# Kernel optimization log

Measured on AMD Instinct MI355X. Metric: run time of the kernel, lower is better.

## Reference

```python
import jax, jax.numpy as jnp
import numpy as np
from jax import lax

HEADS = 4
DIM = 64
GATE_HID = 16


def setup_inputs() -> dict:
    key = jax.random.key(0)
    ks = jax.random.split(key, 12)
    b, c, h, w = 2, DIM, 48, 48
    s = 0.05
    x = jax.random.normal(ks[0], (b, c, h, w), jnp.float32)
    Wqkv = jax.random.normal(ks[1], (3 * c, c), jnp.float32) * s
    bqkv = jax.random.normal(ks[2], (3 * c,), jnp.float32) * s
    Wpos = jax.random.normal(ks[3], (3 * c, 1, 3, 3), jnp.float32) * s
    bpos = jax.random.normal(ks[4], (3 * c,), jnp.float32) * s
    Wg1 = jax.random.normal(ks[5], (GATE_HID, 1), jnp.float32) * 0.5
    bg1 = jax.random.normal(ks[6], (GATE_HID,), jnp.float32) * 0.1
    Wg2 = jax.random.normal(ks[7], (1, GATE_HID), jnp.float32) * 0.5
    bg2 = jax.random.normal(ks[8], (1,), jnp.float32) * 0.1
    Wproj = jax.random.normal(ks[9], (c, c), jnp.float32) * s
    bproj = jax.random.normal(ks[10], (c,), jnp.float32) * s
    return {"x": x, "Wqkv": Wqkv, "bqkv": bqkv, "Wpos": Wpos, "bpos": bpos,
            "Wg1": Wg1, "bg1": bg1, "Wg2": Wg2, "bg2": bg2,
            "Wproj": Wproj, "bproj": bproj}


def _forward(x, Wqkv, bqkv, Wpos, bpos, Wg1, bg1, Wg2, bg2, Wproj, bproj):
    b, c, h, w = x.shape
    n = h * w
    heads = HEADS
    hd = c // heads
    scale = hd ** -0.5
    # qkv 1x1 conv then 3x3 depthwise positional conv
    qkv = jnp.einsum('bchw,oc->bohw', x, Wqkv) + bqkv[None, :, None, None]
    qkv = lax.conv_general_dilated(
        qkv, Wpos, window_strides=(1, 1), padding='SAME',
        feature_group_count=3 * c,
        dimension_numbers=('NCHW', 'OIHW', 'NCHW')) + bpos[None, :, None, None]
    q, k, v = jnp.split(qkv, 3, axis=1)

    def to_heads(t):
        # [b,c,h,w] -> [b,heads,n,hd]
        return t.reshape(b, c, n).transpose(0, 2, 1).reshape(b, n, heads, hd).transpose(0, 2, 1, 3)

    q, k, v = to_heads(q), to_heads(k), to_heads(v)
    attn = jnp.einsum('bhid,bhjd->bhij', q, k) * scale  # [b,heads,n,n]
    prob = jax.nn.softmax(attn, axis=-1)
    entropy = -(prob * jnp.log(jnp.clip(prob, 1e-12))).sum(-1).mean(-1)  # [b,heads]
    # entropy gate: sigmoid(fc2(relu(fc1(e)))) * 0.9 + 0.1
    hgate = jax.nn.relu(entropy[..., None] @ Wg1.T + bg1)  # [b,heads,16]
    ratio = jax.nn.sigmoid(hgate @ Wg2.T + bg2)[..., 0] * 0.9 + 0.1  # [b,heads]
    # dynamic per-(batch,head) top-k along rows via rank threshold
    keep = jnp.clip(jnp.ceil(ratio * n).astype(jnp.int32), 1, n)  # [b,heads]
    sorted_desc = -jnp.sort(-attn, axis=-1)  # [b,heads,n,n]
    idx = jnp.broadcast_to((keep - 1)[:, :, None, None], (b, heads, n, 1))
    thresh = jnp.take_along_axis(sorted_desc, idx, axis=-1)  # [b,heads,n,1]
    sparse = jnp.where(attn >= thresh, attn, -jnp.inf)
    p = jax.nn.softmax(sparse, axis=-1)
    out = jnp.einsum('bhij,bhjd->bhid', p, v)  # [b,heads,n,hd]
    out = out.transpose(0, 2, 1, 3).reshape(b, n, c)
    out = out @ Wproj.T + bproj
    return out.transpose(0, 2, 1).reshape(b, c, h, w)


def reference(x, Wqkv, bqkv, Wpos, bpos, Wg1, bg1, Wg2, bg2, Wproj, bproj):
    return _forward(x, Wqkv, bqkv, Wpos, bpos, Wg1, bg1, Wg2, bg2, Wproj, bproj)
```

## Files before the change

kernel.cpp:

```cpp
#include <hip/hip_runtime.h>
#include <hip/hip_fp16.h>


typedef _Float16 half8_t __attribute__((ext_vector_type(8)));
typedef float floatx4 __attribute__((ext_vector_type(4)));

union HU { unsigned short s; _Float16 h; };
__device__ __forceinline__ _Float16 ubits_h(unsigned short u) {
  HU c; c.s = u; return c.h;
}
__device__ __forceinline__ _Float16 key_h(unsigned k) {
  unsigned short u = (k & 0x8000u) ? (unsigned short)(k & 0x7FFFu)
                                   : (unsigned short)((~k) & 0xFFFFu);
  return ubits_h(u);
}

__device__ __forceinline__ uint2 hist_select_p(const unsigned* h, int lane,
                                               unsigned keepN) {
  uint2 w = ((const uint2*)h)[lane];
  unsigned c0 = w.x & 0xFFFFu, c1 = w.x >> 16;
  unsigned c2 = w.y & 0xFFFFu, c3 = w.y >> 16;
  unsigned inc = c0 + c1 + c2 + c3;
#pragma unroll
  for (int off = 1; off < 64; off <<= 1) {
    unsigned t = __shfl_up(inc, off);
    if (lane >= off) inc += t;
  }
  unsigned total = __shfl(inc, 63);
  unsigned above = total - inc;
  unsigned a3 = above;
  unsigned a2 = a3 + c3;
  unsigned a1 = a2 + c2;
  unsigned a0 = a1 + c1;
  bool has = false;
  unsigned B_l = 0, A_l = 0;
  if (a3 < keepN && a3 + c3 >= keepN) { has = true; B_l = lane * 4 + 3; A_l = a3; }
  else if (a2 < keepN && a2 + c2 >= keepN) { has = true; B_l = lane * 4 + 2; A_l = a2; }
  else if (a1 < keepN && a1 + c1 >= keepN) { has = true; B_l = lane * 4 + 1; A_l = a1; }
  else if (a0 < keepN && a0 + c0 >= keepN) { has = true; B_l = lane * 4 + 0; A_l = a0; }
  unsigned long long m = __ballot(has);
  int src = __ffsll(m) - 1;
  return make_uint2(__shfl(B_l, src), __shfl(A_l, src));
}

__global__ __launch_bounds__(256) void k_qkv(const float* __restrict__ x,
                                             const float* __restrict__ W,
                                             const float* __restrict__ bias,
                                             float* __restrict__ out,
                                             float* __restrict__ ent) {
  if (blockIdx.x == 0 && threadIdx.x < 8) ent[threadIdx.x] = 0.f;
  int blk = blockIdx.x;
  int chunk = blk % 9;
  int og = (blk / 9) % 48;
  int b = blk / (9 * 48);
  int o0 = og * 4;
  int pos = chunk * 256 + threadIdx.x;
  const float* xb = x + b * 64 * 2304 + pos;
  const float* w0 = W + (o0 + 0) * 64;
  const float* w1 = W + (o0 + 1) * 64;
  const float* w2 = W + (o0 + 2) * 64;
  const float* w3 = W + (o0 + 3) * 64;
  float a0 = bias[o0 + 0], a1 = bias[o0 + 1];
  float a2 = bias[o0 + 2], a3 = bias[o0 + 3];
#pragma unroll
  for (int c = 0; c < 64; c++) {
    float xv = xb[c * 2304];
    a0 = fmaf(w0[c], xv, a0);
    a1 = fmaf(w1[c], xv, a1);
    a2 = fmaf(w2[c], xv, a2);
    a3 = fmaf(w3[c], xv, a3);
  }
  out[(b * 192 + o0 + 0) * 2304 + pos] = a0;
  out[(b * 192 + o0 + 1) * 2304 + pos] = a1;
  out[(b * 192 + o0 + 2) * 2304 + pos] = a2;
  out[(b * 192 + o0 + 3) * 2304 + pos] = a3;
}

__global__ __launch_bounds__(256) void k_dw(const float* __restrict__ qkv,
                                            const float* __restrict__ Wpos,
                                            const float* __restrict__ bpos,
                                            _Float16* __restrict__ q2,
                                            _Float16* __restrict__ k2,
                                            _Float16* __restrict__ vt) {
  __shared__ float smem[8][384];
  int blk = blockIdx.x;
  int chunk = blk % 9;
  int half = (blk / 9) % 2;
  int sel = (blk / 18) % 3;
  int head = (blk / 54) % 4;
  int b = blk / 216;
  int chbase = sel * 64 + head * 16 + half * 8;
  int bh = b * 4 + head;
  int tid = threadIdx.x;
  int p0 = chunk * 256;
  int baserow = p0 / 48;
  int rA = min(max(baserow - 1, 0), 40);

  const float* src = qkv + (size_t)(b * 192 + chbase) * 2304;
#pragma unroll
  for (int l = 0; l < 12; l++) {
    int idx = tid + l * 256;
    int ch = idx / 384;
    int off = idx - ch * 384;
    int rr = off / 48;
    int cc = off - rr * 48;
    smem[ch][off] = src[(size_t)ch * 2304 + (rA + rr) * 48 + cc];
  }
  __syncthreads();

  int pos = p0 + tid;
  int yy = pos / 48, xx = pos - yy * 48;
  int ry = yy - rA;
  float accv[8];
#pragma unroll
  for (int d = 0; d < 8; d++) {
    const float* w = Wpos + (chbase + d) * 9;
    float a = bpos[chbase + d];
#pragma unroll
    for (int dy = -1; dy <= 1; dy++) {
      int y2 = yy + dy;
      if ((unsigned)y2 < 48u) {
#pragma unroll
        for (int dx = -1; dx <= 1; dx++) {
          int x2 = xx + dx;
          if ((unsigned)x2 < 48u)
            a = fmaf(w[(dy + 1) * 3 + (dx + 1)], smem[d][(ry + dy) * 48 + x2],
                     a);
        }
      }
    }
    accv[d] = a;
  }

  if (sel == 2) {
#pragma unroll
    for (int d = 0; d < 8; d++)
      vt[((size_t)bh * 16 + half * 8 + d) * 2304 + pos] = (_Float16)accv[d];
  } else {
    _Float16 h1[8], h2[8];
#pragma unroll
    for (int d = 0; d < 8; d++) {
      float a = (sel == 0) ? accv[d] * 0.25f : accv[d];
      h1[d] = (_Float16)a;
      h2[d] = (_Float16)(a - (float)h1[d]);
    }
    _Float16* dst = ((sel == 0) ? q2 : k2) + ((size_t)bh * 2304 + pos) * 32;
    *(uint4*)(dst + half * 8) = *(uint4*)&h1[0];
    *(uint4*)(dst + 16 + half * 8) = *(uint4*)&h2[0];
  }
}

template <bool STORE>
__global__ __launch_bounds__(256) void k_ent_t(const _Float16* __restrict__ q2,
                                               const _Float16* __restrict__ k2,
                                               float* __restrict__ ent,
                                               _Float16* __restrict__ lgH) {
  __shared__ __align__(16) _Float16 tBuf[4][16][72];
  __shared__ float sWv[4][16], uWv[4][16];

  int blk = blockIdx.x;
  int rowtile = blk % 144;
  int bh = blk / 144;
  int row0 = rowtile * 16;
  int tid = threadIdx.x, lane = tid & 63, wave = tid >> 6;
  int m16 = lane & 15, quad = lane >> 4;

  const half8_t* q2v =
      (const half8_t*)(q2 + ((size_t)bh * 2304 + row0 + m16) * 32);
  half8_t A1 = q2v[quad];
  half8_t zh = {};
  half8_t A2 = (lane < 32) ? A1 : zh;
  const half8_t* kbase = (const half8_t*)(k2 + (size_t)bh * 2304 * 32);

  float s[4] = {0.f, 0.f, 0.f, 0.f}, u[4] = {0.f, 0.f, 0.f, 0.f};
  for (int g = 0; g < 9; g++) {
#pragma unroll
    for (int tt = 0; tt < 4; tt++) {
      int t = g * 4 + tt;
      int col = wave * 576 + t * 16 + m16;
      const half8_t* kk = kbase + (size_t)col * 4;
      half8_t b1 = kk[quad & 1];
      half8_t b2 = kk[2 + (quad & 1)];
      floatx4 acc = {};
      acc = __builtin_amdgcn_mfma_f32_16x16x32_f16(A2, b2, acc, 0, 0, 0);
      acc = __builtin_amdgcn_mfma_f32_16x16x32_f16(A1, b1, acc, 0, 0, 0);
#pragma unroll
      for (int i = 0; i < 4; i++) {
        if (STORE) tBuf[wave][quad * 4 + i][tt * 16 + m16] = (_Float16)acc[i];
        float e = __expf(acc[i]);
        s[i] += e;
        u[i] = fmaf(acc[i], e, u[i]);
      }
    }
    if (STORE) {
      __syncthreads();
      int rb = lane >> 3, seg = lane & 7;
#pragma unroll
      for (int it = 0; it < 2; it++) {
        int rr = it * 8 + rb;
        uint4 vv = *(const uint4*)&tBuf[wave][rr][seg * 8];
        *(uint4*)(lgH + ((size_t)bh * 2304 + row0 + rr) * 2304 + wave * 576 +
                  g * 64 + seg * 8) = vv;
      }
      __syncthreads();
    }
  }
#pragma unroll
  for (int off = 1; off < 16; off <<= 1) {
#pragma unroll
    for (int i = 0; i < 4; i++) {
      s[i] += __shfl_xor(s[i], off);
      u[i] += __shfl_xor(u[i], off);
    }
  }
  if (m16 == 0) {
#pragma unroll
    for (int i = 0; i < 4; i++) {
      sWv[wave][quad * 4 + i] = s[i];
      uWv[wave][quad * 4 + i] = u[i];
    }
  }
  __syncthreads();
  if (tid < 16) {
    float S = sWv[0][tid] + sWv[1][tid] + sWv[2][tid] + sWv[3][tid];
    float U = uWv[0][tid] + uWv[1][tid] + uWv[2][tid] + uWv[3][tid];
    float er = __logf(S) - U / S;
    er += __shfl_xor(er, 1);
    er += __shfl_xor(er, 2);
    er += __shfl_xor(er, 4);
    er += __shfl_xor(er, 8);
    if (tid == 0) atomicAdd(&ent[bh], er);
  }
}

__global__ __launch_bounds__(512, 2) void k_attn_f(
    const _Float16* __restrict__ q2, const _Float16* __restrict__ k2,
    const _Float16* __restrict__ vt, const float* __restrict__ ent,
    const float* __restrict__ Wg1, const float* __restrict__ bg1,
    const float* __restrict__ Wg2, const float* __restrict__ bg2,
    float* __restrict__ oh) {
  __shared__ __align__(16) _Float16 lg[16 * 2304];
  __shared__ unsigned hist[8][128];
  __shared__ float sS[16];

  int blk = blockIdx.x;
  int bh = blk & 7;
  int tile = blk >> 3;
  int row0 = tile * 16;
  int tid = threadIdx.x, lane = tid & 63, wave = tid >> 6;
  int m16 = lane & 15, quad = lane >> 4;
  char* lgc = (char*)lg;

  float eAvg = ent[bh] * (1.f / 2304.f);
  float gacc = bg2[0];
#pragma unroll
  for (int i = 0; i < 16; i++) {
    float h = fmaxf(fmaf(eAvg, Wg1[i], bg1[i]), 0.f);
    gacc = fmaf(h, Wg2[i], gacc);
  }
  float ratio = 0.9f / (1.f + __expf(-gacc)) + 0.1f;
  int kp = (int)ceilf(ratio * 2304.f);
  unsigned keep = (unsigned)min(max(kp, 1), 2304);

  {
    const half8_t* q2v =
        (const half8_t*)(q2 + ((size_t)bh * 2304 + row0 + m16) * 32);
    half8_t A1 = q2v[quad];
    half8_t zh = {};
    half8_t A2 = (lane < 32) ? A1 : zh;
    const half8_t* kbase = (const half8_t*)(k2 + (size_t)bh * 2304 * 32);
#pragma unroll 2
    for (int t = 0; t < 18; t++) {
      int col = wave * 288 + t * 16 + m16;
      const half8_t* kk = kbase + (size_t)col * 4;
      half8_t b1 = kk[quad & 1];
      half8_t b2 = kk[2 + (quad & 1)];
      floatx4 acc = {};
      acc = __builtin_amdgcn_mfma_f32_16x16x32_f16(A2, b2, acc, 0, 0, 0);
      acc = __builtin_amdgcn_mfma_f32_16x16x32_f16(A1, b1, acc, 0, 0, 0);
#pragma unroll
      for (int i = 0; i < 4; i++) {
        int row = quad * 4 + i;
        *(_Float16*)(lgc + row * 4608 +
                     ((col * 2) ^ (((row >> 2) & 3) << 5))) =
            (_Float16)acc[i];
      }
    }
  }
  __syncthreads();

#pragma unroll 1
  for (int rr = 0; rr < 2; rr++) {
    int r = wave * 2 + rr;
    char* rb = lgc + r * 4608;
    int sw = ((r >> 2) & 3) << 5;
    uint4 q0 = *(const uint4*)(rb + ((lane * 16) ^ sw));
    uint4 q1 = *(const uint4*)(rb + ((1024 + lane * 16) ^ sw));
    uint4 q2r = *(const uint4*)(rb + ((2048 + lane * 16) ^ sw));
    uint4 q3 = *(const uint4*)(rb + ((3072 + lane * 16) ^ sw));
    uint2 q4 = *(const uint2*)(rb + ((4096 + lane * 8) ^ sw));
    unsigned wb[18] = {q0.x, q0.y, q0.z, q0.w, q1.x, q1.y, q1.z, q1.w,
                       q2r.x, q2r.y, q2r.z, q2r.w, q3.x, q3.y, q3.z, q3.w,
                       q4.x, q4.y};
    unsigned kb[18];
#pragma unroll
    for (int i = 0; i < 18; i++)
      kb[i] = wb[i] ^ (((wb[i] >> 15) & 0x00010001u) * 0x7FFFu + 0x80008000u);

    unsigned* h = hist[wave];
    h[lane] = 0u;
    h[lane + 64] = 0u;
#pragma unroll
    for (int i = 0; i < 18; i++) {
      unsigned b1 = (kb[i] >> 8) & 0xFFu;
      unsigned b2 = kb[i] >> 24;
      atomicAdd(&h[b1 >> 1], 1u << ((b1 & 1) << 4));
      atomicAdd(&h[b2 >> 1], 1u << ((b2 & 1) << 4));
    }
    uint2 s1 = hist_select_p(h, lane, keep);
    unsigned B = s1.x;
    unsigned keep2 = keep - s1.y;

    h[lane] = 0u;
    h[lane + 64] = 0u;
#pragma unroll
    for (int i = 0; i < 18; i++) {
      unsigned klo = kb[i] & 0xFFFFu;
      unsigned khi = kb[i] >> 16;
      if ((klo >> 8) == B) {
        unsigned lb = klo & 0xFFu;
        atomicAdd(&h[lb >> 1], 1u << ((lb & 1) << 4));
      }
      if ((khi >> 8) == B) {
        unsigned lb = khi & 0xFFu;
        atomicAdd(&h[lb >> 1], 1u << ((lb & 1) << 4));
      }
    }
    uint2 s2 = hist_select_p(h, lane, keep2);
    _Float16 th_h = key_h((B << 8) | s2.x);

    float sp = 0.f;
#pragma unroll
    for (int g = 0; g < 4; g++) {
      uint4 o;
      unsigned ow[4];
#pragma unroll
      for (int wj = 0; wj < 4; wj++) {
        unsigned w = wb[g * 4 + wj];
        _Float16 hlo = ubits_h((unsigned short)(w & 0xFFFFu));
        _Float16 hhi = ubits_h((unsigned short)(w >> 16));
        float plo = (hlo >= th_h) ? __expf((float)hlo) : 0.f;
        float phi = (hhi >= th_h) ? __expf((float)hhi) : 0.f;
        __half2 hp = __floats2half2_rn(plo, phi);
        ow[wj] = *(unsigned*)&hp;
        if (wj == 0) sp += ((plo + phi));
      }
      o.x = ow[0]; o.y = ow[1]; o.z = ow[2]; o.w = ow[3];
      *(uint4*)(rb + (((g * 1024) + lane * 16) ^ sw)) = o;
      {
        _Float16 h2a = ubits_h((unsigned short)(wb[g * 4 + 1] & 0xFFFFu));
        _Float16 h2b = ubits_h((unsigned short)(wb[g * 4 + 1] >> 16));
        _Float16 h3a = ubits_h((unsigned short)(wb[g * 4 + 2] & 0xFFFFu));
        _Float16 h3b = ubits_h((unsigned short)(wb[g * 4 + 2] >> 16));
        _Float16 h4a = ubits_h((unsigned short)(wb[g * 4 + 3] & 0xFFFFu));
        _Float16 h4b = ubits_h((unsigned short)(wb[g * 4 + 3] >> 16));
        float p2 = (h2a >= th_h) ? __expf((float)h2a) : 0.f;
        float p3 = (h2b >= th_h) ? __expf((float)h2b) : 0.f;
        float p4 = (h3a >= th_h) ? __expf((float)h3a) : 0.f;
        float p5 = (h3b >= th_h) ? __expf((float)h3b) : 0.f;
        float p6 = (h4a >= th_h) ? __expf((float)h4a) : 0.f;
        float p7 = (h4b >= th_h) ? __expf((float)h4b) : 0.f;
        sp += (p2 + p3);
        sp += (p4 + p5) + (p6 + p7);
      }
    }
    {
      _Float16 h0 = ubits_h((unsigned short)(wb[16] & 0xFFFFu));
      _Float16 h1 = ubits_h((unsigned short)(wb[16] >> 16));
      _Float16 h2 = ubits_h((unsigned short)(wb[17] & 0xFFFFu));
      _Float16 h3 = ubits_h((unsigned short)(wb[17] >> 16));
      float p0 = (h0 >= th_h) ? __expf((float)h0) : 0.f;
      float p1 = (h1 >= th_h) ? __expf((float)h1) : 0.f;
      float p2 = (h2 >= th_h) ? __expf((float)h2) : 0.f;
      float p3 = (h3 >= th_h) ? __expf((float)h3) : 0.f;
      sp += (p0 + p1) + (p2 + p3);
      uint2 o;
      __half2 hp0 = __floats2half2_rn(p0, p1); o.x = *(unsigned*)&hp0;
      __half2 hp1 = __floats2half2_rn(p2, p3); o.y = *(unsigned*)&hp1;
      *(uint2*)(rb + ((4096 + lane * 8) ^ sw)) = o;
    }
#pragma unroll
    for (int off = 1; off < 64; off <<= 1) sp += __shfl_xor(sp, off);
    if (lane == 0) sS[r] = sp;
  }
  __syncthreads();

  floatx4 acc = {};
  if (wave < 4) {
    const _Float16* vrow = vt + ((size_t)bh * 16 + m16) * 2304;
    const char* pr = lgc + m16 * 4608;
    int sw2 = ((m16 >> 2) & 3) << 5;
    int jb0 = wave * 576 + quad * 8;
#pragma unroll 6
    for (int t = 0; t < 18; t++) {
      int jb = jb0 + t * 32;
      half8_t a2 = *(const half8_t*)(pr + ((jb * 2) ^ sw2));
      half8_t b2 = *(const half8_t*)&vrow[jb];
      acc = __builtin_amdgcn_mfma_f32_16x16x32_f16(a2, b2, acc, 0, 0, 0);
    }
  }
  __syncthreads();
  float* red = (float*)lg;
  if (wave < 4) {
#pragma unroll
    for (int i = 0; i < 4; i++)
      red[wave * 256 + (quad * 4 + i) * 16 + m16] = acc[i];
  }
  __syncthreads();
  if (tid < 256) {
    int r = tid >> 4;
    float s2 = red[0 * 256 + tid] + red[1 * 256 + tid] +
               red[2 * 256 + tid] + red[3 * 256 + tid];
    int d = tid & 15;
    oh[((size_t)(bh * 2304 + row0 + r)) * 16 + d] = s2 / sS[r];
  }
}

__global__ __launch_bounds__(256) void k_proj(const float* __restrict__ oh,
                                              const float* __restrict__ Wp,
                                              const float* __restrict__ bp,
                                              float* __restrict__ out) {
  int blk = blockIdx.x;
  int chunk = blk % 9;
  int cog = (blk / 9) % 16;
  int b = blk / (9 * 16);
  int co0 = cog * 4;
  int pos = chunk * 256 + threadIdx.x;
  float a0 = bp[co0 + 0], a1 = bp[co0 + 1], a2 = bp[co0 + 2], a3 = bp[co0 + 3];
#pragma unroll
  for (int head = 0; head < 4; head++) {
    const float4* op =
        (const float4*)(oh + ((size_t)((b * 4 + head) * 2304 + pos)) * 16);
#pragma unroll
    for (int p = 0; p < 4; p++) {
      float4 o4 = op[p];
#pragma unroll
      for (int i = 0; i < 4; i++) {
        const float* wr = Wp + (co0 + i) * 64 + head * 16 + p * 4;
        float* ai = (i == 0) ? &a0 : ((i == 1) ? &a1 : ((i == 2) ? &a2 : &a3));
        *ai = fmaf(wr[0], o4.x, *ai);
        *ai = fmaf(wr[1], o4.y, *ai);
        *ai = fmaf(wr[2], o4.z, *ai);
        *ai = fmaf(wr[3], o4.w, *ai);
      }
    }
  }
  out[(b * 64 + co0 + 0) * 2304 + pos] = a0;
  out[(b * 64 + co0 + 1) * 2304 + pos] = a1;
  out[(b * 64 + co0 + 2) * 2304 + pos] = a2;
  out[(b * 64 + co0 + 3) * 2304 + pos] = a3;
}

extern "C" void kernel_launch(void* const* d_in, const int* in_sizes, int n_in,
                              void* d_out, int out_size, void* d_ws,
                              size_t ws_size, hipStream_t stream) {
  const float* x    = (const float*)d_in[0];
  const float* Wqkv = (const float*)d_in[1];
  const float* bqkv = (const float*)d_in[2];
  const float* Wpos = (const float*)d_in[3];
  const float* bpos = (const float*)d_in[4];
  const float* Wg1  = (const float*)d_in[5];
  const float* bg1  = (const float*)d_in[6];
  const float* Wg2  = (const float*)d_in[7];
  const float* bg2  = (const float*)d_in[8];
  const float* Wpr  = (const float*)d_in[9];
  const float* bpr  = (const float*)d_in[10];
  float* out = (float*)d_out;

  char* base = (char*)d_ws;
  float* qkv_raw = (float*)base;
  float* oh = qkv_raw + 884736;
  float* ent = oh + 294912;
  _Float16* q2 = (_Float16*)(ent + 8);
  _Float16* k2 = q2 + 589824;
  _Float16* vt = k2 + 589824;

  hipLaunchKernelGGL(k_qkv, dim3(2 * 48 * 9), dim3(256), 0, stream,
                     x, Wqkv, bqkv, qkv_raw, ent);
  hipLaunchKernelGGL(k_dw, dim3(432), dim3(256), 0, stream,
                     qkv_raw, Wpos, bpos, q2, k2, vt);
  hipLaunchKernelGGL((k_ent_t<false>), dim3(8 * 144), dim3(256), 0, stream,
                     q2, k2, ent, (_Float16*)nullptr);
  hipLaunchKernelGGL(k_attn_f, dim3(1152), dim3(512), 0, stream,
                     q2, k2, vt, ent, Wg1, bg1, Wg2, bg2, oh);
  hipLaunchKernelGGL(k_proj, dim3(2 * 16 * 9), dim3(256), 0, stream,
                     oh, Wpr, bpr, out);
}
```

Measured before the change: 200.9 us.

## Shrink attention tile to 8 rows per block to raise occupancy

```diff
diff --git a/kernel.cpp b/kernel.cpp
--- a/kernel.cpp
+++ b/kernel.cpp
@@ -233,23 +233,23 @@
   }
 }
 
-__global__ __launch_bounds__(512, 2) void k_attn_f(
+__global__ __launch_bounds__(512, 6) void k_attn_f(
     const _Float16* __restrict__ q2, const _Float16* __restrict__ k2,
     const _Float16* __restrict__ vt, const float* __restrict__ ent,
     const float* __restrict__ Wg1, const float* __restrict__ bg1,
     const float* __restrict__ Wg2, const float* __restrict__ bg2,
     float* __restrict__ oh) {
-  __shared__ __align__(16) _Float16 lg[16 * 2304];
+  __shared__ __align__(16) _Float16 lg[8 * 2320];
   __shared__ unsigned hist[8][128];
-  __shared__ float sS[16];
+  __shared__ float sS[8];
+  __shared__ __align__(16) float redSh[8][64];
 
   int blk = blockIdx.x;
   int bh = blk & 7;
   int tile = blk >> 3;
-  int row0 = tile * 16;
+  int row0 = tile * 8;
   int tid = threadIdx.x, lane = tid & 63, wave = tid >> 6;
   int m16 = lane & 15, quad = lane >> 4;
-  char* lgc = (char*)lg;
 
   float eAvg = ent[bh] * (1.f / 2304.f);
   float gacc = bg2[0];
@@ -264,7 +264,7 @@
 
   {
     const half8_t* q2v =
-        (const half8_t*)(q2 + ((size_t)bh * 2304 + row0 + m16) * 32);
+        (const half8_t*)(q2 + ((size_t)bh * 2304 + row0 + (m16 & 7)) * 32);
     half8_t A1 = q2v[quad];
     half8_t zh = {};
     half8_t A2 = (lane < 32) ? A1 : zh;
@@ -278,27 +278,23 @@
       floatx4 acc = {};
       acc = __builtin_amdgcn_mfma_f32_16x16x32_f16(A2, b2, acc, 0, 0, 0);
       acc = __builtin_amdgcn_mfma_f32_16x16x32_f16(A1, b1, acc, 0, 0, 0);
-#pragma unroll
-      for (int i = 0; i < 4; i++) {
-        int row = quad * 4 + i;
-        *(_Float16*)(lgc + row * 4608 +
-                     ((col * 2) ^ (((row >> 2) & 3) << 5))) =
-            (_Float16)acc[i];
+      if (quad < 2) {
+#pragma unroll
+        for (int i = 0; i < 4; i++)
+          lg[(quad * 4 + i) * 2320 + col] = (_Float16)acc[i];
       }
     }
   }
   __syncthreads();
 
-#pragma unroll 1
-  for (int rr = 0; rr < 2; rr++) {
-    int r = wave * 2 + rr;
-    char* rb = lgc + r * 4608;
-    int sw = ((r >> 2) & 3) << 5;
-    uint4 q0 = *(const uint4*)(rb + ((lane * 16) ^ sw));
-    uint4 q1 = *(const uint4*)(rb + ((1024 + lane * 16) ^ sw));
-    uint4 q2r = *(const uint4*)(rb + ((2048 + lane * 16) ^ sw));
-    uint4 q3 = *(const uint4*)(rb + ((3072 + lane * 16) ^ sw));
-    uint2 q4 = *(const uint2*)(rb + ((4096 + lane * 8) ^ sw));
+  {
+    char* rb = (char*)lg + wave * 4640;
+    const uint4* s4 = (const uint4*)rb;
+    uint4 q0 = s4[lane];
+    uint4 q1 = s4[lane + 64];
+    uint4 q2r = s4[lane + 128];
+    uint4 q3 = s4[lane + 192];
+    uint2 q4 = *(const uint2*)(rb + 4096 + lane * 8);
     unsigned wb[18] = {q0.x, q0.y, q0.z, q0.w, q1.x, q1.y, q1.z, q1.w,
                        q2r.x, q2r.y, q2r.z, q2r.w, q3.x, q3.y, q3.z, q3.w,
                        q4.x, q4.y};
@@ -340,6 +336,7 @@
     _Float16 th_h = key_h((B << 8) | s2.x);
 
     float sp = 0.f;
+    uint4* prow4 = (uint4*)rb;
 #pragma unroll
     for (int g = 0; g < 4; g++) {
       uint4 o;
@@ -356,7 +353,7 @@
         if (wj == 0) sp += ((plo + phi));
       }
       o.x = ow[0]; o.y = ow[1]; o.z = ow[2]; o.w = ow[3];
-      *(uint4*)(rb + (((g * 1024) + lane * 16) ^ sw)) = o;
+      prow4[lane + g * 64] = o;
       {
         _Float16 h2a = ubits_h((unsigned short)(wb[g * 4 + 1] & 0xFFFFu));
         _Float16 h2b = ubits_h((unsigned short)(wb[g * 4 + 1] >> 16));
@@ -387,42 +384,40 @@
       uint2 o;
       __half2 hp0 = __floats2half2_rn(p0, p1); o.x = *(unsigned*)&hp0;
       __half2 hp1 = __floats2half2_rn(p2, p3); o.y = *(unsigned*)&hp1;
-      *(uint2*)(rb + ((4096 + lane * 8) ^ sw)) = o;
+      *(uint2*)(rb + 4096 + lane * 8) = o;
     }
 #pragma unroll
     for (int off = 1; off < 64; off <<= 1) sp += __shfl_xor(sp, off);
-    if (lane == 0) sS[r] = sp;
+    if (lane == 0) sS[wave] = sp;
   }
   __syncthreads();
 
-  floatx4 acc = {};
-  if (wave < 4) {
+  {
+    int g = wave >> 2;
+    int jq = wave & 3;
     const _Float16* vrow = vt + ((size_t)bh * 16 + m16) * 2304;
-    const char* pr = lgc + m16 * 4608;
-    int sw2 = ((m16 >> 2) & 3) << 5;
-    int jb0 = wave * 576 + quad * 8;
+    const _Float16* prow = lg + (size_t)(g * 4 + (m16 & 3)) * 2320;
+    int jb0 = jq * 576 + quad * 8;
+    floatx4 acc = {};
 #pragma unroll 6
     for (int t = 0; t < 18; t++) {
       int jb = jb0 + t * 32;
-      half8_t a2 = *(const half8_t*)(pr + ((jb * 2) ^ sw2));
+      half8_t a2 = *(const half8_t*)&prow[jb];
       half8_t b2 = *(const half8_t*)&vrow[jb];
       acc = __builtin_amdgcn_mfma_f32_16x16x32_f16(a2, b2, acc, 0, 0, 0);
     }
+    if (lane < 16) {
+      *(floatx4*)&redSh[wave][m16 * 4] = acc;
+    }
   }
   __syncthreads();
-  float* red = (float*)lg;
-  if (wave < 4) {
-#pragma unroll
-    for (int i = 0; i < 4; i++)
-      red[wave * 256 + (quad * 4 + i) * 16 + m16] = acc[i];
-  }
-  __syncthreads();
-  if (tid < 256) {
-    int r = tid >> 4;
-    float s2 = red[0 * 256 + tid] + red[1 * 256 + tid] +
-               red[2 * 256 + tid] + red[3 * 256 + tid];
-    int d = tid & 15;
-    oh[((size_t)(bh * 2304 + row0 + r)) * 16 + d] = s2 / sS[r];
+  if (tid < 128) {
+    int g = tid >> 6, idx = tid & 63;
+    int r = idx & 3, d = idx >> 2;
+    float s2 = redSh[g * 4 + 0][d * 4 + r] + redSh[g * 4 + 1][d * 4 + r] +
+               redSh[g * 4 + 2][d * 4 + r] + redSh[g * 4 + 3][d * 4 + r];
+    oh[((size_t)(bh * 2304 + row0 + g * 4 + r)) * 16 + d] =
+        s2 / sS[g * 4 + r];
   }
 }
 
@@ -491,7 +486,7 @@
                      qkv_raw, Wpos, bpos, q2, k2, vt);
   hipLaunchKernelGGL((k_ent_t<false>), dim3(8 * 144), dim3(256), 0, stream,
                      q2, k2, ent, (_Float16*)nullptr);
-  hipLaunchKernelGGL(k_attn_f, dim3(1152), dim3(512), 0, stream,
+  hipLaunchKernelGGL(k_attn_f, dim3(2304), dim3(512), 0, stream,
                      q2, k2, vt, ent, Wg1, bg1, Wg2, bg2, oh);
   hipLaunchKernelGGL(k_proj, dim3(2 * 16 * 9), dim3(256), 0, stream,
                      oh, Wpr, bpr, out);
```

New measurement: 229.4 us. 14.2% more time.
